# Performance work log

Hardware: AMD Instinct MI355X
Metric: run time of the kernel (lower is better)

Reference implementation:

```python
import jax, jax.numpy as jnp
import numpy as np

U, I, A, D, NC = 20000, 15000, 2048, 64, 2048
N = U + I
E_AU, E_AI, E_UI, E_R = 300000, 300000, 300000, 60000


def setup_inputs() -> dict:
    keys = iter(jax.random.split(jax.random.key(0), 128))
    def rn(shape, s=0.05):
        return jax.random.normal(next(keys), shape, jnp.float32) * s
    def ru(shape):
        return jax.random.uniform(next(keys), shape, dtype=jnp.float32)
    def ri(shape, mx):
        return jax.random.randint(next(keys), shape, 0, mx)
    d = {}
    for nm in ("feature1", "feature2", "feature3", "weight1", "weight2", "weight3", "weight4", "weight5"):
        d[nm] = rn((N, D))
    d["W_review1"] = rn((D, D)); d["W_review2"] = rn((D, D))
    for i in range(1, 7):
        d["rating_emb%d" % i] = rn((5, D))
    d["W_aspect"] = rn((D, D)); d["W_aspect2"] = rn((D, D))
    d["W_count_user"] = rn((NC, D)); d["b_count_user"] = rn((D,))
    d["W_count_item"] = rn((NC, D)); d["b_count_item"] = rn((D,))
    d["aspect_fe"] = rn((A, D)); d["aspect_cau"] = rn((A, D)); d["aspect_cai"] = rn((A, D))
    d["user_cau"] = rn((U, D)); d["user_cui"] = rn((U, D))
    d["item_cai"] = rn((I, D)); d["item_ciu"] = rn((I, D))
    for i in range(1, 6):
        d["user_cui%d" % i] = rn((U, D)); d["item_ciu%d" % i] = rn((I, D))
    d["user_mask"] = ru((U,)); d["item_mask"] = ru((I,))
    d["user_aspect_count"] = ru((U, NC)); d["item_aspect_count"] = ru((I, NC))
    d["ui_review"] = rn((E_UI, D), 1.0); d["iu_review"] = rn((E_UI, D), 1.0)
    for i in range(1, 6):
        d["ui%d_review" % i] = rn((E_R, D), 1.0); d["iu%d_review" % i] = rn((E_R, D), 1.0)
    d["au_src"] = ri((E_AU,), A); d["au_dst"] = ri((E_AU,), U)
    d["ai_src"] = ri((E_AI,), A); d["ai_dst"] = ri((E_AI,), I)
    d["ui_src"] = ri((E_UI,), U); d["ui_dst"] = ri((E_UI,), I); d["ui_rating"] = ri((E_UI,), 5)
    d["iu_src"] = ri((E_UI,), I); d["iu_dst"] = ri((E_UI,), U); d["iu_rating"] = ri((E_UI,), 5)
    for i in range(1, 6):
        d["ui%d_src" % i] = ri((E_R,), U); d["ui%d_dst" % i] = ri((E_R,), I)
        d["iu%d_src" % i] = ri((E_R,), I); d["iu%d_dst" % i] = ri((E_R,), U)
    return d


def reference(feature1, feature2, feature3, weight1, weight2, weight3, weight4, weight5,
              W_review1, W_review2, rating_emb1, rating_emb2, rating_emb3, rating_emb4,
              rating_emb5, rating_emb6, W_aspect, W_aspect2, W_count_user, b_count_user,
              W_count_item, b_count_item, aspect_fe, aspect_cau, aspect_cai,
              user_cau, user_cui, user_cui1, user_cui2, user_cui3, user_cui4, user_cui5,
              user_mask, user_aspect_count, item_cai, item_ciu, item_ciu1, item_ciu2,
              item_ciu3, item_ciu4, item_ciu5, item_mask, item_aspect_count,
              ui_review, iu_review, ui1_review, ui2_review, ui3_review, ui4_review, ui5_review,
              iu1_review, iu2_review, iu3_review, iu4_review, iu5_review,
              au_src, au_dst, ai_src, ai_dst, ui_src, ui_dst, ui_rating,
              iu_src, iu_dst, iu_rating,
              ui1_src, ui1_dst, ui2_src, ui2_dst, ui3_src, ui3_dst, ui4_src, ui4_dst,
              ui5_src, ui5_dst, iu1_src, iu1_dst, iu2_src, iu2_dst, iu3_src, iu3_dst,
              iu4_src, iu4_dst, iu5_src, iu5_dst):
    sig = jax.nn.sigmoid
    cat = jnp.concatenate
    def seg(m, idx, n):
        return jax.ops.segment_sum(m, idx, num_segments=n)
    u_fe1, i_fe1 = feature1[:U], feature1[U:]
    u_fe2, i_fe2 = feature2[:U], feature2[U:]
    u_fe3, i_fe3 = feature3[:U], feature3[U:]
    mu = user_mask[:, None]; mi = item_mask[:, None]
    # --- aspect -> user/item (dropout = identity, eval mode) ---
    f_fe = aspect_fe @ W_aspect        # [A, D]
    f_fe2 = aspect_fe @ W_aspect2
    h_u = seg((f_fe * aspect_cau)[au_src], au_dst, U)
    h_i = seg((f_fe2 * aspect_cai)[ai_src], ai_dst, I)
    from_a_u = mu * (h_u * user_cau) + (1.0 - mu) * u_fe2
    from_a_i = mi * (h_i * item_cai) + (1.0 - mi) * i_fe2
    # --- rating-gated pass over from_a ---
    h_i = seg((from_a_u * user_cui)[ui_src] * sig(rating_emb1[ui_rating]), ui_dst, I)
    h_u = seg((from_a_i * item_ciu)[iu_src] * sig(rating_emb2[iu_rating]), iu_dst, U)
    user_item_senti_fe = cat([h_u * user_cui, h_i * item_ciu], 0)
    # --- aspect-count pass ---
    ac_u = user_aspect_count @ W_count_user + b_count_user
    ac_i = item_aspect_count @ W_count_item + b_count_item
    ac_u = mu * (ac_u * user_cau) + (1.0 - mu) * u_fe3
    ac_i = mi * (ac_i * item_cai) + (1.0 - mi) * i_fe3
    h_i = seg((ac_u * user_cui)[ui_src] * sig(rating_emb3[ui_rating]), ui_dst, I)
    h_u = seg((ac_i * item_ciu)[iu_src] * sig(rating_emb4[iu_rating]), iu_dst, U)
    user_item_count_fe = cat([h_u * user_cui, h_i * item_ciu], 0)
    # --- per-rating relations ---
    ws = [weight1, weight2, weight3, weight4, weight5]
    cuis = [user_cui1, user_cui2, user_cui3, user_cui4, user_cui5]
    cius = [item_ciu1, item_ciu2, item_ciu3, item_ciu4, item_ciu5]
    ui_e = [(ui1_src, ui1_dst, ui1_review), (ui2_src, ui2_dst, ui2_review),
            (ui3_src, ui3_dst, ui3_review), (ui4_src, ui4_dst, ui4_review),
            (ui5_src, ui5_dst, ui5_review)]
    iu_e = [(iu1_src, iu1_dst, iu1_review), (iu2_src, iu2_dst, iu2_review),
            (iu3_src, iu3_dst, iu3_review), (iu4_src, iu4_dst, iu4_review),
            (iu5_src, iu5_dst, iu5_review)]
    fe5_parts, re_parts = [], []
    for w, cui_k, ciu_k, (us, ud, urv), (isrc, idst, irv) in zip(ws, cuis, cius, ui_e, iu_e):
        re_ui = urv @ W_review1        # [E_R, D]
        re_iu = irv @ W_review2
        wu, wi = w[:U], w[U:]
        h_ik = seg((wu[us] + re_ui) * cui_k[us], ud, I)
        h_uk = seg((wi[isrc] + re_iu) * ciu_k[isrc], idst, U)
        fe5_parts.append(cat([h_uk * cui_k, h_ik * ciu_k], 0))
        h_ir = seg(re_ui * cui_k[us], ud, I)
        h_ur = seg(re_iu * ciu_k[isrc], idst, U)
        re_parts.append(cat([h_ur * cui_k, h_ir * ciu_k], 0))
    user_item_fe5 = cat(fe5_parts, -1)   # [N, 5*D]
    user_item_re = cat(re_parts, -1)
    # --- base-feature pass ---
    h_i = seg((u_fe1 * user_cui)[ui_src] * sig(rating_emb5[ui_rating]), ui_dst, I)
    h_u = seg((i_fe1 * item_ciu)[iu_src] * sig(rating_emb6[iu_rating]), iu_dst, U)
    user_item_fe = cat([h_u * user_cui, h_i * item_ciu], 0)
    return (user_item_senti_fe, user_item_count_fe, user_item_fe, user_item_fe5, user_item_re)
```

## Files before the change

kernel.cpp:

```cpp
#include <hip/hip_runtime.h>
#include <cstddef>

#define U_CNT 20000
#define I_CNT 15000
#define N_CNT 35000
#define A_CNT 2048
#define NC_K  2048
#define EAU   300000
#define EUI   300000
#define ER    60000
#define NLIST 14

__device__ __forceinline__ float4 ld4(const float* p){ return *reinterpret_cast<const float4*>(p); }
__device__ __forceinline__ void st4(float* p, float4 v){ *reinterpret_cast<float4*>(p) = v; }
__device__ __forceinline__ float4 mul4(float4 a, float4 b){ return make_float4(a.x*b.x, a.y*b.y, a.z*b.z, a.w*b.w); }
__device__ __forceinline__ float4 add4(float4 a, float4 b){ return make_float4(a.x+b.x, a.y+b.y, a.z+b.z, a.w+b.w); }
__device__ __forceinline__ float4 fmas4(float s, float4 b, float4 c){
  return make_float4(fmaf(s,b.x,c.x), fmaf(s,b.y,c.y), fmaf(s,b.z,c.z), fmaf(s,b.w,c.w));
}
__device__ __forceinline__ unsigned short f2bf(float x){
  unsigned u = __float_as_uint(x);
  u += 0x7fffu + ((u >> 16) & 1u);
  return (unsigned short)(u >> 16);
}
__device__ __forceinline__ float bf2f(unsigned short s){
  return __uint_as_float(((unsigned)s) << 16);
}

__device__ __forceinline__ void gemm_core(
    const float* __restrict__ A, int lda, int M, int r0,
    const float* __restrict__ W, int k0base, int kcount,
    float* __restrict__ smem, float4* accs)
{
  float (*As)[36] = (float (*)[36])smem;
  float (*Ws)[64] = (float (*)[64])(smem + 64*36);
  const int t = threadIdx.x;
  const int ty = t >> 4, tx = t & 15;
  float4 acc0 = make_float4(0,0,0,0), acc1 = acc0, acc2 = acc0, acc3 = acc0;
  for (int k0 = k0base; k0 < k0base + kcount; k0 += 32) {
    __syncthreads();
    #pragma unroll
    for (int i = 0; i < 2; ++i) {
      int f = t + i*256;
      int row = f >> 3, caa = (f & 7) << 2;
      float4 v = make_float4(0.f,0.f,0.f,0.f);
      int r = r0 + row;
      if (r < M) v = ld4(&A[(size_t)r*lda + k0 + caa]);
      st4(&As[row][caa], v);
      int kk = f >> 4, cb = (f & 15) << 2;
      st4(&Ws[kk][cb], ld4(&W[(size_t)(k0+kk)*64 + cb]));
    }
    __syncthreads();
    #pragma unroll
    for (int kk = 0; kk < 32; kk += 4) {
      float4 a0 = ld4(&As[ty*4+0][kk]);
      float4 a1 = ld4(&As[ty*4+1][kk]);
      float4 a2 = ld4(&As[ty*4+2][kk]);
      float4 a3 = ld4(&As[ty*4+3][kk]);
      float a0v[4] = {a0.x,a0.y,a0.z,a0.w};
      float a1v[4] = {a1.x,a1.y,a1.z,a1.w};
      float a2v[4] = {a2.x,a2.y,a2.z,a2.w};
      float a3v[4] = {a3.x,a3.y,a3.z,a3.w};
      #pragma unroll
      for (int j = 0; j < 4; ++j) {
        float4 wv = ld4(&Ws[kk+j][tx<<2]);
        acc0 = fmas4(a0v[j], wv, acc0);
        acc1 = fmas4(a1v[j], wv, acc1);
        acc2 = fmas4(a2v[j], wv, acc2);
        acc3 = fmas4(a3v[j], wv, acc3);
      }
    }
  }
  accs[0]=acc0; accs[1]=acc1; accs[2]=acc2; accs[3]=acc3;
}

__global__ __launch_bounds__(256) void fill_m1(int4* __restrict__ p, int n4)
{
  int gid = blockIdx.x*256 + threadIdx.x;
  if (gid < n4) p[gid] = make_int4(-1,-1,-1,-1);
}

struct Mega1Args {
  int e_sp, e_build, e_k64a, e_k64r, e_fe1c;
  const float* emb[6]; float* sigt;
  const float* f1; const float* cui; const float* ciu; float* fe1c;
  const float* spA[2]; const float* spW[2]; int spM[2];
  const float* spBias[2]; const float* spMask[2];
  const float* spCa[2]; const float* spFe[2]; const float* spCui[2]; float* spOut[2];
  const float* aA[2]; const float* aW[2]; const float* aMul[2]; float* aC[2];
  const float* rA[10]; const float* rW[10]; unsigned short* rC[10];
  const int* bsrc[NLIST]; const int* bdst[NLIST];
  const int* rat2; const int* rat3;
  int2* node[NLIST]; int* head[NLIST];
};

__global__ __launch_bounds__(256, 8) void mega1(Mega1Args a)
{
  __shared__ float smem[64*36 + 32*64];
  int b = blockIdx.x, t = threadIdx.x;
  const int ty = t >> 4, tx = t & 15;
  if (b < a.e_sp) {
    int side = (b >= 313);
    int bx = side ? (b - 313) : b;
    int M = a.spM[side];
    int r0 = bx*64;
    float4 accs[4];
    gemm_core(a.spA[side], NC_K, M, r0, a.spW[side], 0, NC_K, smem, accs);
    float4 bv = ld4(&a.spBias[side][tx<<2]);
    #pragma unroll
    for (int i = 0; i < 4; ++i) {
      int r = r0 + ty*4 + i;
      if (r < M) {
        size_t o = (size_t)r*64 + (tx<<2);
        float4 v = add4(accs[i], bv);
        float m = a.spMask[side][r], im = 1.f - m;
        float4 cav = ld4(&a.spCa[side][o]), fev = ld4(&a.spFe[side][o]), cv = ld4(&a.spCui[side][o]);
        st4(&a.spOut[side][o], make_float4((m*(v.x*cav.x) + im*fev.x)*cv.x,
                                           (m*(v.y*cav.y) + im*fev.y)*cv.y,
                                           (m*(v.z*cav.z) + im*fev.z)*cv.z,
                                           (m*(v.w*cav.w) + im*fev.w)*cv.w));
      }
    }
    return;
  }
  if (b < a.e_build) {
    int local = b - a.e_sp;
    int li, bx;
    if (local < 4*1172) { li = local/1172; bx = local%1172; }
    else { int l2 = local - 4*1172; li = 4 + l2/235; bx = l2%235; }
    int E = (li < 4) ? EAU : ER;
    int i = bx*256 + t;
    if (i < E) {
      int d = a.bdst[li][i];
      int pay = a.bsrc[li][i];
      if (li == 2) pay |= a.rat2[i] << 20;
      else if (li == 3) pay |= a.rat3[i] << 20;
      int prev = atomicExch(&a.head[li][d], i);
      a.node[li][i] = make_int2(prev, pay);
    }
    return;
  }
  if (b < a.e_k64a) {
    int local = b - a.e_build;
    int z = local/32, bx = local%32;
    int r0 = bx*64;
    float4 accs[4];
    gemm_core(a.aA[z], 64, A_CNT, r0, a.aW[z], 0, 64, smem, accs);
    const float* mulp = a.aMul[z];
    float* C = a.aC[z];
    #pragma unroll
    for (int i = 0; i < 4; ++i) {
      int r = r0 + ty*4 + i;
      size_t o = (size_t)r*64 + (tx<<2);
      st4(&C[o], mul4(accs[i], ld4(&mulp[o])));
    }
    return;
  }
  if (b < a.e_k64r) {
    int local = b - a.e_k64a;
    int z = local/938, bx = local%938;
    int r0 = bx*64;
    float4 accs[4];
    gemm_core(a.rA[z], 64, ER, r0, a.rW[z], 0, 64, smem, accs);
    unsigned short* C = a.rC[z];
    #pragma unroll
    for (int i = 0; i < 4; ++i) {
      int r = r0 + ty*4 + i;
      if (r < ER) {
        ushort4 o4;
        o4.x = f2bf(accs[i].x); o4.y = f2bf(accs[i].y);
        o4.z = f2bf(accs[i].z); o4.w = f2bf(accs[i].w);
        *reinterpret_cast<ushort4*>(&C[(size_t)r*64 + (tx<<2)]) = o4;
      }
    }
    return;
  }
  if (b < a.e_fe1c) {
    int gid = (b - a.e_k64r)*256 + t;
    if (gid < N_CNT*16) {
      int n = gid >> 4, q = (gid & 15) << 2;
      size_t o = (size_t)n*64 + q;
      float4 v = ld4(&a.f1[o]);
      float4 c = (n < U_CNT) ? ld4(&a.cui[o]) : ld4(&a.ciu[(size_t)(n-U_CNT)*64 + q]);
      st4(&a.fe1c[o], mul4(v, c));
    }
    return;
  }
  {
    int gid = (b - a.e_fe1c)*256 + t;
    if (gid < 6*320) {
      int k = gid/320, j = gid%320;
      a.sigt[gid] = 1.f/(1.f + __expf(-a.emb[k][j]));
    }
  }
}

#define FE5Z 10
struct Mega2Args {
  const int* f_head[FE5Z]; const int2* f_node[FE5Z];
  const unsigned short* f_re[FE5Z]; const float* f_w[FE5Z]; const float* f_cui[FE5Z];
  const float* f_cmul[FE5Z]; float* f_outA[FE5Z]; float* f_outB[FE5Z]; int f_n[FE5Z];
  const int* gb_head[2]; const int2* gb_node[2];
  const float* gb_msg[2]; const float* gb_mask[2]; const float* gb_ca[2];
  const float* gb_fe[2]; const float* gb_cui[2]; float* gb_out[2]; int gb_n[2];
};

__global__ __launch_bounds__(256) void mega2(Mega2Args a)
{
  int b = blockIdx.x, t = threadIdx.x;
  int q = (t & 15) << 2;
  const int B_FE5 = 5*1250 + 5*938;
  if (b < B_FE5) {
    int z, bx;
    if (b < 6250) { z = 2*(b/1250) + 1; bx = b%1250; }
    else { int l2 = b - 6250; z = 2*(l2/938); bx = l2%938; }
    int d = bx*16 + (t >> 4);
    if (d >= a.f_n[z]) return;
    const int2* __restrict__ node = a.f_node[z];
    const unsigned short* __restrict__ re = a.f_re[z];
    const float* __restrict__ w = a.f_w[z];
    const float* __restrict__ cuiS = a.f_cui[z];
    float4 a0 = make_float4(0,0,0,0), a1 = a0;
    for (int cur = a.f_head[z][d]; cur >= 0; ) {
      int2 nd = node[cur];
      int e = cur;
      cur = nd.x;
      int s = nd.y;
      ushort4 r4 = *reinterpret_cast<const ushort4*>(&re[(size_t)e*64 + q]);
      float4 rv = make_float4(bf2f(r4.x), bf2f(r4.y), bf2f(r4.z), bf2f(r4.w));
      float4 cv = ld4(&cuiS[(size_t)s*64 + q]);
      float4 wv = ld4(&w[(size_t)s*64 + q]);
      a0 = add4(a0, mul4(add4(wv, rv), cv));
      a1 = add4(a1, mul4(rv, cv));
    }
    float4 c = ld4(&a.f_cmul[z][(size_t)d*64 + q]);
    size_t o = (size_t)d*320 + q;
    st4(&a.f_outA[z][o], mul4(a0, c));
    st4(&a.f_outB[z][o], mul4(a1, c));
    return;
  }
  int local = b - B_FE5;
  {
    int side = (local >= 1250);
    int bx = side ? (local - 1250) : local;
    int d = bx*16 + (t >> 4);
    if (d >= a.gb_n[side]) return;
    const int2* __restrict__ node = a.gb_node[side];
    const float* __restrict__ msg = a.gb_msg[side];
    float4 acc = make_float4(0,0,0,0);
    for (int cur = a.gb_head[side][d]; cur >= 0; ) {
      int2 nd = node[cur];
      cur = nd.x;
      acc = add4(acc, ld4(&msg[(size_t)nd.y*64 + q]));
    }
    size_t o = (size_t)d*64 + q;
    float m = a.gb_mask[side][d], im = 1.f - m;
    float4 cav = ld4(&a.gb_ca[side][o]), fev = ld4(&a.gb_fe[side][o]), cv = ld4(&a.gb_cui[side][o]);
    st4(&a.gb_out[side][o], make_float4((m*(acc.x*cav.x) + im*fev.x)*cv.x,
                                        (m*(acc.y*cav.y) + im*fev.y)*cv.y,
                                        (m*(acc.z*cav.z) + im*fev.z)*cv.z,
                                        (m*(acc.w*cav.w) + im*fev.w)*cv.w));
  }
}

struct Mega3Args {
  int e_g3i;
  const int* head[2]; const int2* node[2];
  const float* msgA[2]; const float* msgB[2]; const float* msgC[2];
  const float* sigA[2]; const float* sigB[2]; const float* sigC[2];
  const float* cmul[2]; float* outA[2]; float* outB[2]; float* outC[2]; int n[2];
};

__global__ __launch_bounds__(256) void mega3(Mega3Args a)
{
  int b = blockIdx.x, t = threadIdx.x;
  int side = (b >= a.e_g3i);
  int bx = side ? (b - a.e_g3i) : b;
  int d = bx*16 + (t >> 4);
  if (d >= a.n[side]) return;
  int q = (t & 15) << 2;
  const int2* __restrict__ node = a.node[side];
  const float* __restrict__ msgA = a.msgA[side];
  const float* __restrict__ msgB = a.msgB[side];
  const float* __restrict__ msgC = a.msgC[side];
  const float* __restrict__ sigA = a.sigA[side];
  const float* __restrict__ sigB = a.sigB[side];
  const float* __restrict__ sigC = a.sigC[side];
  float4 a0 = make_float4(0,0,0,0), a1 = a0, a2 = a0;
  for (int cur = a.head[side][d]; cur >= 0; ) {
    int2 nd = node[cur];
    cur = nd.x;
    int s = nd.y & 0xFFFFF;
    int r = nd.y >> 20;
    size_t so = (size_t)s*64 + q;
    int ro = r*64 + q;
    a0 = add4(a0, mul4(ld4(&msgA[so]), ld4(&sigA[ro])));
    a1 = add4(a1, mul4(ld4(&msgB[so]), ld4(&sigB[ro])));
    a2 = add4(a2, mul4(ld4(&msgC[so]), ld4(&sigC[ro])));
  }
  size_t o = (size_t)d*64 + q;
  float4 c = ld4(&a.cmul[side][o]);
  st4(&a.outA[side][o], mul4(a0, c));
  st4(&a.outB[side][o], mul4(a1, c));
  st4(&a.outC[side][o], mul4(a2, c));
}

extern "C" void kernel_launch(void* const* d_in, const int* in_sizes, int n_in,
                              void* d_out, int out_size, void* d_ws, size_t ws_size,
                              hipStream_t stream)
{
  (void)in_sizes; (void)n_in; (void)out_size; (void)ws_size;
  auto F = [&](int i){ return (const float*)d_in[i]; };
  auto Ix = [&](int i){ return (const int*)d_in[i]; };

  const float* feature1 = F(0);
  const float* feature2 = F(1);
  const float* feature3 = F(2);
  const float* weightK[5]   = {F(3),F(4),F(5),F(6),F(7)};
  const float* W_review1 = F(8);
  const float* W_review2 = F(9);
  const float* rating_emb[6] = {F(10),F(11),F(12),F(13),F(14),F(15)};
  const float* W_aspect  = F(16);
  const float* W_aspect2 = F(17);
  const float* W_count_user = F(18);
  const float* b_count_user = F(19);
  const float* W_count_item = F(20);
  const float* b_count_item = F(21);
  const float* aspect_fe  = F(22);
  const float* aspect_cau = F(23);
  const float* aspect_cai = F(24);
  const float* user_cau = F(25);
  const float* user_cui = F(26);
  const float* item_cai = F(27);
  const float* item_ciu = F(28);
  const float* user_cuiK[5] = {F(29),F(31),F(33),F(35),F(37)};
  const float* item_ciuK[5] = {F(30),F(32),F(34),F(36),F(38)};
  const float* user_mask = F(39);
  const float* item_mask = F(40);
  const float* user_aspect_count = F(41);
  const float* item_aspect_count = F(42);
  const float* uiK_review[5] = {F(45),F(47),F(49),F(51),F(53)};
  const float* iuK_review[5] = {F(46),F(48),F(50),F(52),F(54)};
  const int* au_src = Ix(55); const int* au_dst = Ix(56);
  const int* ai_src = Ix(57); const int* ai_dst = Ix(58);
  const int* ui_src = Ix(59); const int* ui_dst = Ix(60); const int* ui_rating = Ix(61);
  const int* iu_src = Ix(62); const int* iu_dst = Ix(63); const int* iu_rating = Ix(64);
  const int* uiK_src[5] = {Ix(65),Ix(69),Ix(73),Ix(77),Ix(81)};
  const int* uiK_dst[5] = {Ix(66),Ix(70),Ix(74),Ix(78),Ix(82)};
  const int* iuK_src[5] = {Ix(67),Ix(71),Ix(75),Ix(79),Ix(83)};
  const int* iuK_dst[5] = {Ix(68),Ix(72),Ix(76),Ix(80),Ix(84)};

  float* out  = (float*)d_out;
  float* out2 = out + (size_t)N_CNT*64;
  float* out3 = out + 2*(size_t)N_CNT*64;
  float* out4 = out + 3*(size_t)N_CNT*64;
  float* out5 = out + 8*(size_t)N_CNT*64;

  float* ws = (float*)d_ws;
  size_t off = 0;
  auto alloc = [&](size_t n){ float* p = ws + off; off += (n + 3) & ~(size_t)3; return p; };
  float* sigt   = alloc(6*320);
  float* msg_au = alloc((size_t)A_CNT*64);
  float* msg_ai = alloc((size_t)A_CNT*64);
  float* h_u_a  = alloc((size_t)U_CNT*64);
  float* h_i_a  = alloc((size_t)I_CNT*64);
  float* g_u    = alloc((size_t)U_CNT*64);
  float* g_i    = alloc((size_t)I_CNT*64);
  float* fe1c   = alloc((size_t)N_CNT*64);

  const size_t reUSH = (size_t)ER*64;
  float* rebf = alloc(10*reUSH/2);
  unsigned short* rebb[10];
  for (int j = 0; j < 10; ++j) rebb[j] = (unsigned short*)rebf + (size_t)j*reUSH;

  const int* l_src[NLIST] = {au_src, ai_src, ui_src, iu_src,
                             uiK_src[0],uiK_src[1],uiK_src[2],uiK_src[3],uiK_src[4],
                             iuK_src[0],iuK_src[1],iuK_src[2],iuK_src[3],iuK_src[4]};
  const int* l_dst[NLIST] = {au_dst, ai_dst, ui_dst, iu_dst,
                             uiK_dst[0],uiK_dst[1],uiK_dst[2],uiK_dst[3],uiK_dst[4],
                             iuK_dst[0],iuK_dst[1],iuK_dst[2],iuK_dst[3],iuK_dst[4]};
  int l_E[NLIST]    = {EAU,EAU,EUI,EUI, ER,ER,ER,ER,ER, ER,ER,ER,ER,ER};
  int l_nseg[NLIST] = {U_CNT,I_CNT,I_CNT,U_CNT, I_CNT,I_CNT,I_CNT,I_CNT,I_CNT,
                       U_CNT,U_CNT,U_CNT,U_CNT,U_CNT};

  int* ibase = (int*)(ws + off);
  int* lhead[NLIST]; int2* lnode[NLIST];
  size_t io = 0;
  for (int l = 0; l < NLIST; ++l) { lhead[l] = ibase + io; io += l_nseg[l]; }
  size_t head_ints = io;
  for (int l = 0; l < NLIST; ++l) { lnode[l] = (int2*)(ibase + io); io += 2*(size_t)l_E[l]; }
  off += (io + 3) & ~(size_t)3;

  fill_m1<<<(int)((head_ints/4 + 255)/256), 256, 0, stream>>>((int4*)ibase, (int)(head_ints/4));

  Mega1Args a1;
  const int B_SP    = 313 + 235;
  const int B_BUILD = 4*1172 + 10*235;
  const int B_K64A  = 64;
  const int B_K64R  = 10*938;
  const int B_FE1C  = (N_CNT*16 + 255)/256;
  const int B_SIG   = 8;
  a1.e_sp    = B_SP;
  a1.e_build = B_SP + B_BUILD;
  a1.e_k64a  = a1.e_build + B_K64A;
  a1.e_k64r  = a1.e_k64a + B_K64R;
  a1.e_fe1c  = a1.e_k64r + B_FE1C;
  for (int k = 0; k < 6; ++k) a1.emb[k] = rating_emb[k];
  a1.sigt = sigt;
  a1.f1 = feature1; a1.cui = user_cui; a1.ciu = item_ciu; a1.fe1c = fe1c;
  a1.spA[0] = user_aspect_count; a1.spW[0] = W_count_user; a1.spM[0] = U_CNT;
  a1.spBias[0] = b_count_user; a1.spMask[0] = user_mask;
  a1.spCa[0] = user_cau; a1.spFe[0] = feature3; a1.spCui[0] = user_cui; a1.spOut[0] = g_u;
  a1.spA[1] = item_aspect_count; a1.spW[1] = W_count_item; a1.spM[1] = I_CNT;
  a1.spBias[1] = b_count_item; a1.spMask[1] = item_mask;
  a1.spCa[1] = item_cai; a1.spFe[1] = feature3 + (size_t)U_CNT*64; a1.spCui[1] = item_ciu; a1.spOut[1] = g_i;
  a1.aA[0]=aspect_fe; a1.aW[0]=W_aspect;  a1.aMul[0]=aspect_cau; a1.aC[0]=msg_au;
  a1.aA[1]=aspect_fe; a1.aW[1]=W_aspect2; a1.aMul[1]=aspect_cai; a1.aC[1]=msg_ai;
  for (int k = 0; k < 5; ++k) {
    a1.rA[k]   = uiK_review[k]; a1.rW[k]   = W_review1; a1.rC[k]   = rebb[k];
    a1.rA[5+k] = iuK_review[k]; a1.rW[5+k] = W_review2; a1.rC[5+k] = rebb[5+k];
  }
  for (int l = 0; l < NLIST; ++l) {
    a1.bsrc[l]=l_src[l]; a1.bdst[l]=l_dst[l];
    a1.node[l]=lnode[l]; a1.head[l]=lhead[l];
  }
  a1.rat2 = ui_rating; a1.rat3 = iu_rating;
  mega1<<<a1.e_fe1c + B_SIG, 256, 0, stream>>>(a1);

  Mega2Args a2;
  for (int k = 0; k < 5; ++k) {
    int z = 2*k;
    a2.f_head[z]=lhead[4+k]; a2.f_node[z]=lnode[4+k];
    a2.f_re[z]=rebb[k]; a2.f_w[z]=weightK[k]; a2.f_cui[z]=user_cuiK[k]; a2.f_cmul[z]=item_ciuK[k];
    a2.f_outA[z]=out4 + (size_t)U_CNT*320 + (size_t)k*64;
    a2.f_outB[z]=out5 + (size_t)U_CNT*320 + (size_t)k*64;
    a2.f_n[z]=I_CNT;
    a2.f_head[z+1]=lhead[9+k]; a2.f_node[z+1]=lnode[9+k];
    a2.f_re[z+1]=rebb[5+k]; a2.f_w[z+1]=weightK[k] + (size_t)U_CNT*64;
    a2.f_cui[z+1]=item_ciuK[k]; a2.f_cmul[z+1]=user_cuiK[k];
    a2.f_outA[z+1]=out4 + (size_t)k*64;
    a2.f_outB[z+1]=out5 + (size_t)k*64;
    a2.f_n[z+1]=U_CNT;
  }
  a2.gb_head[0]=lhead[0]; a2.gb_node[0]=lnode[0]; a2.gb_msg[0]=msg_au;
  a2.gb_mask[0]=user_mask; a2.gb_ca[0]=user_cau; a2.gb_fe[0]=feature2;
  a2.gb_cui[0]=user_cui; a2.gb_out[0]=h_u_a; a2.gb_n[0]=U_CNT;
  a2.gb_head[1]=lhead[1]; a2.gb_node[1]=lnode[1]; a2.gb_msg[1]=msg_ai;
  a2.gb_mask[1]=item_mask; a2.gb_ca[1]=item_cai; a2.gb_fe[1]=feature2 + (size_t)U_CNT*64;
  a2.gb_cui[1]=item_ciu; a2.gb_out[1]=h_i_a; a2.gb_n[1]=I_CNT;
  const int B_M2 = (5*1250 + 5*938) + 2188;
  mega2<<<B_M2, 256, 0, stream>>>(a2);

  Mega3Args a3;
  a3.e_g3i = 938;
  a3.head[0]=lhead[2]; a3.node[0]=lnode[2];
  a3.msgA[0]=h_u_a; a3.msgB[0]=g_u; a3.msgC[0]=fe1c;
  a3.sigA[0]=sigt + 0*320; a3.sigB[0]=sigt + 2*320; a3.sigC[0]=sigt + 4*320;
  a3.cmul[0]=item_ciu;
  a3.outA[0]=out + (size_t)U_CNT*64; a3.outB[0]=out2 + (size_t)U_CNT*64; a3.outC[0]=out3 + (size_t)U_CNT*64;
  a3.n[0]=I_CNT;
  a3.head[1]=lhead[3]; a3.node[1]=lnode[3];
  a3.msgA[1]=h_i_a; a3.msgB[1]=g_i; a3.msgC[1]=fe1c + (size_t)U_CNT*64;
  a3.sigA[1]=sigt + 1*320; a3.sigB[1]=sigt + 3*320; a3.sigC[1]=sigt + 5*320;
  a3.cmul[1]=user_cui;
  a3.outA[1]=out; a3.outB[1]=out2; a3.outC[1]=out3;
  a3.n[1]=U_CNT;
  mega3<<<938 + 1250, 256, 0, stream>>>(a3);
}
```

Measured before the change: 481.1 us.

## Split-K the aspect-count GEMM with bf16 partials reduced in mega2

The user/item aspect-count GEMM (K=2048) is now split along K into up to four chunks, each computed by its own block in mega1. Each block writes a bf16 partial result to workspace. A new section of mega2 sums the partials, adds the bias and applies the mask/ca/fe/cui epilogue. This adds parallelism to the long-K GEMM blocks, which were likely the critical path in mega1. The cost is extra workspace traffic, bf16 rounding of the partial sums, and more blocks in mega2.

```diff
diff --git a/kernel.cpp b/kernel.cpp
--- a/kernel.cpp
+++ b/kernel.cpp
@@ -81,12 +81,10 @@
 }
 
 struct Mega1Args {
-  int e_sp, e_build, e_k64a, e_k64r, e_fe1c;
+  int e_sp, e_build, e_k64a, e_k64r, e_fe1c, split;
   const float* emb[6]; float* sigt;
   const float* f1; const float* cui; const float* ciu; float* fe1c;
-  const float* spA[2]; const float* spW[2]; int spM[2];
-  const float* spBias[2]; const float* spMask[2];
-  const float* spCa[2]; const float* spFe[2]; const float* spCui[2]; float* spOut[2];
+  const float* spA[2]; const float* spW[2]; unsigned short* spPart[2]; int spM[2];
   const float* aA[2]; const float* aW[2]; const float* aMul[2]; float* aC[2];
   const float* rA[10]; const float* rW[10]; unsigned short* rC[10];
   const int* bsrc[NLIST]; const int* bdst[NLIST];
@@ -100,25 +98,24 @@
   int b = blockIdx.x, t = threadIdx.x;
   const int ty = t >> 4, tx = t & 15;
   if (b < a.e_sp) {
-    int side = (b >= 313);
-    int bx = side ? (b - 313) : b;
+    int nb0 = a.split*313;
+    int side, sp, bx;
+    if (b < nb0) { side = 0; sp = b/313; bx = b%313; }
+    else         { int b2 = b-nb0; side = 1; sp = b2/235; bx = b2%235; }
     int M = a.spM[side];
     int r0 = bx*64;
+    int kchunk = NC_K/a.split;
     float4 accs[4];
-    gemm_core(a.spA[side], NC_K, M, r0, a.spW[side], 0, NC_K, smem, accs);
-    float4 bv = ld4(&a.spBias[side][tx<<2]);
+    gemm_core(a.spA[side], NC_K, M, r0, a.spW[side], sp*kchunk, kchunk, smem, accs);
+    unsigned short* base = a.spPart[side] + (size_t)sp * M * 64;
     #pragma unroll
     for (int i = 0; i < 4; ++i) {
       int r = r0 + ty*4 + i;
       if (r < M) {
-        size_t o = (size_t)r*64 + (tx<<2);
-        float4 v = add4(accs[i], bv);
-        float m = a.spMask[side][r], im = 1.f - m;
-        float4 cav = ld4(&a.spCa[side][o]), fev = ld4(&a.spFe[side][o]), cv = ld4(&a.spCui[side][o]);
-        st4(&a.spOut[side][o], make_float4((m*(v.x*cav.x) + im*fev.x)*cv.x,
-                                           (m*(v.y*cav.y) + im*fev.y)*cv.y,
-                                           (m*(v.z*cav.z) + im*fev.z)*cv.z,
-                                           (m*(v.w*cav.w) + im*fev.w)*cv.w));
+        ushort4 o4;
+        o4.x = f2bf(accs[i].x); o4.y = f2bf(accs[i].y);
+        o4.z = f2bf(accs[i].z); o4.w = f2bf(accs[i].w);
+        *reinterpret_cast<ushort4*>(&base[(size_t)r*64 + (tx<<2)]) = o4;
       }
     }
     return;
@@ -197,12 +194,16 @@
 
 #define FE5Z 10
 struct Mega2Args {
+  int split;
   const int* f_head[FE5Z]; const int2* f_node[FE5Z];
   const unsigned short* f_re[FE5Z]; const float* f_w[FE5Z]; const float* f_cui[FE5Z];
   const float* f_cmul[FE5Z]; float* f_outA[FE5Z]; float* f_outB[FE5Z]; int f_n[FE5Z];
   const int* gb_head[2]; const int2* gb_node[2];
   const float* gb_msg[2]; const float* gb_mask[2]; const float* gb_ca[2];
   const float* gb_fe[2]; const float* gb_cui[2]; float* gb_out[2]; int gb_n[2];
+  const unsigned short* part[2]; int M[2];
+  const float* bias[2]; const float* mask[2];
+  const float* ca[2]; const float* fe[2]; const float* cui[2]; float* outb[2];
 };
 
 __global__ __launch_bounds__(256) void mega2(Mega2Args a)
@@ -240,7 +241,7 @@
     return;
   }
   int local = b - B_FE5;
-  {
+  if (local < 2188) {
     int side = (local >= 1250);
     int bx = side ? (local - 1250) : local;
     int d = bx*16 + (t >> 4);
@@ -260,7 +261,27 @@
                                         (m*(acc.y*cav.y) + im*fev.y)*cv.y,
                                         (m*(acc.z*cav.z) + im*fev.z)*cv.z,
                                         (m*(acc.w*cav.w) + im*fev.w)*cv.w));
-  }
+    return;
+  }
+  local -= 2188;
+  int side = (local >= 1250);
+  int gid = (side ? (local - 1250) : local)*256 + t;
+  int M = a.M[side];
+  if (gid >= M*16) return;
+  int n = gid >> 4;
+  float4 acc = ld4(&a.bias[side][q]);
+  const unsigned short* part = a.part[side];
+  for (int s = 0; s < a.split; ++s) {
+    ushort4 p4 = *reinterpret_cast<const ushort4*>(&part[((size_t)s*M + n)*64 + q]);
+    acc = add4(acc, make_float4(bf2f(p4.x), bf2f(p4.y), bf2f(p4.z), bf2f(p4.w)));
+  }
+  size_t o = (size_t)n*64 + q;
+  float m = a.mask[side][n], im = 1.f - m;
+  float4 cav = ld4(&a.ca[side][o]), fev = ld4(&a.fe[side][o]), cv = ld4(&a.cui[side][o]);
+  st4(&a.outb[side][o], make_float4((m*(acc.x*cav.x) + im*fev.x)*cv.x,
+                                    (m*(acc.y*cav.y) + im*fev.y)*cv.y,
+                                    (m*(acc.z*cav.z) + im*fev.z)*cv.z,
+                                    (m*(acc.w*cav.w) + im*fev.w)*cv.w));
 }
 
 struct Mega3Args {
@@ -309,7 +330,7 @@
                               void* d_out, int out_size, void* d_ws, size_t ws_size,
                               hipStream_t stream)
 {
-  (void)in_sizes; (void)n_in; (void)out_size; (void)ws_size;
+  (void)in_sizes; (void)n_in; (void)out_size;
   auto F = [&](int i){ return (const float*)d_in[i]; };
   auto Ix = [&](int i){ return (const int*)d_in[i]; };
 
@@ -391,10 +412,15 @@
   for (int l = 0; l < NLIST; ++l) { lnode[l] = (int2*)(ibase + io); io += 2*(size_t)l_E[l]; }
   off += (io + 3) & ~(size_t)3;
 
+  int SPLIT = 4;
+  while (SPLIT > 1 && (off + ((size_t)SPLIT*N_CNT*64 + 1)/2) * 4 > ws_size) SPLIT >>= 1;
+  unsigned short* part_u = (unsigned short*)(ws + off);
+  unsigned short* part_i = part_u + (size_t)SPLIT*U_CNT*64;
+
   fill_m1<<<(int)((head_ints/4 + 255)/256), 256, 0, stream>>>((int4*)ibase, (int)(head_ints/4));
 
   Mega1Args a1;
-  const int B_SP    = 313 + 235;
+  const int B_SP    = SPLIT*313 + SPLIT*235;
   const int B_BUILD = 4*1172 + 10*235;
   const int B_K64A  = 64;
   const int B_K64R  = 10*938;
@@ -405,15 +431,12 @@
   a1.e_k64a  = a1.e_build + B_K64A;
   a1.e_k64r  = a1.e_k64a + B_K64R;
   a1.e_fe1c  = a1.e_k64r + B_FE1C;
+  a1.split   = SPLIT;
   for (int k = 0; k < 6; ++k) a1.emb[k] = rating_emb[k];
   a1.sigt = sigt;
   a1.f1 = feature1; a1.cui = user_cui; a1.ciu = item_ciu; a1.fe1c = fe1c;
-  a1.spA[0] = user_aspect_count; a1.spW[0] = W_count_user; a1.spM[0] = U_CNT;
-  a1.spBias[0] = b_count_user; a1.spMask[0] = user_mask;
-  a1.spCa[0] = user_cau; a1.spFe[0] = feature3; a1.spCui[0] = user_cui; a1.spOut[0] = g_u;
-  a1.spA[1] = item_aspect_count; a1.spW[1] = W_count_item; a1.spM[1] = I_CNT;
-  a1.spBias[1] = b_count_item; a1.spMask[1] = item_mask;
-  a1.spCa[1] = item_cai; a1.spFe[1] = feature3 + (size_t)U_CNT*64; a1.spCui[1] = item_ciu; a1.spOut[1] = g_i;
+  a1.spA[0] = user_aspect_count; a1.spW[0] = W_count_user; a1.spPart[0] = part_u; a1.spM[0] = U_CNT;
+  a1.spA[1] = item_aspect_count; a1.spW[1] = W_count_item; a1.spPart[1] = part_i; a1.spM[1] = I_CNT;
   a1.aA[0]=aspect_fe; a1.aW[0]=W_aspect;  a1.aMul[0]=aspect_cau; a1.aC[0]=msg_au;
   a1.aA[1]=aspect_fe; a1.aW[1]=W_aspect2; a1.aMul[1]=aspect_cai; a1.aC[1]=msg_ai;
   for (int k = 0; k < 5; ++k) {
@@ -428,6 +451,7 @@
   mega1<<<a1.e_fe1c + B_SIG, 256, 0, stream>>>(a1);
 
   Mega2Args a2;
+  a2.split = SPLIT;
   for (int k = 0; k < 5; ++k) {
     int z = 2*k;
     a2.f_head[z]=lhead[4+k]; a2.f_node[z]=lnode[4+k];
@@ -448,7 +472,11 @@
   a2.gb_head[1]=lhead[1]; a2.gb_node[1]=lnode[1]; a2.gb_msg[1]=msg_ai;
   a2.gb_mask[1]=item_mask; a2.gb_ca[1]=item_cai; a2.gb_fe[1]=feature2 + (size_t)U_CNT*64;
   a2.gb_cui[1]=item_ciu; a2.gb_out[1]=h_i_a; a2.gb_n[1]=I_CNT;
-  const int B_M2 = (5*1250 + 5*938) + 2188;
+  a2.part[0]=part_u; a2.M[0]=U_CNT; a2.bias[0]=b_count_user; a2.mask[0]=user_mask;
+  a2.ca[0]=user_cau; a2.fe[0]=feature3; a2.cui[0]=user_cui; a2.outb[0]=g_u;
+  a2.part[1]=part_i; a2.M[1]=I_CNT; a2.bias[1]=b_count_item; a2.mask[1]=item_mask;
+  a2.ca[1]=item_cai; a2.fe[1]=feature3 + (size_t)U_CNT*64; a2.cui[1]=item_ciu; a2.outb[1]=g_i;
+  const int B_M2 = (5*1250 + 5*938) + 2188 + 2188;
   mega2<<<B_M2, 256, 0, stream>>>(a2);
 
   Mega3Args a3;
```

After: 445.3 us. -7.4%, faster.
